# Optimization experiments

Hardware: AMD Instinct MI355X
Metric: run time of the kernel (lower is better)

Reference implementation:

```python
import jax, jax.numpy as jnp
import numpy as np

ND, NS = 50000, 30000
FD = FS = 256
H = 256
E = 1000000
EL = 200000


def _lin_init(key, fan_in, fan_out):
    # torch Linear default: U(-1/sqrt(fan_in), 1/sqrt(fan_in)) for W and b
    kw, kb = jax.random.split(key)
    bound = 1.0 / np.sqrt(fan_in)
    W = jax.random.uniform(kw, (fan_in, fan_out), jnp.float32, -bound, bound)
    b = jax.random.uniform(kb, (fan_out,), jnp.float32, -bound, bound)
    return W, b


def setup_inputs() -> dict:
    key = jax.random.key(0)
    ks = jax.random.split(key, 16)
    x_drug = jax.random.normal(ks[0], (ND, FD), jnp.float32)
    x_disease = jax.random.normal(ks[1], (NS, FS), jnp.float32)
    edge_src = jax.random.randint(ks[2], (E,), 0, ND, jnp.int64)
    edge_dst = jax.random.randint(ks[3], (E,), 0, NS, jnp.int64)
    label_row = jax.random.randint(ks[4], (EL,), 0, ND, jnp.int64)
    label_col = jax.random.randint(ks[5], (EL,), 0, NS, jnp.int64)
    # SAGEConv params per layer per edge type: lin_l (on aggregated src, with bias),
    # lin_r (on dst root, no bias). Edge types: ds = drug->disease, sd = disease->drug (rev).
    Wl1_ds, bl1_ds = _lin_init(ks[6], FD, H)
    Wr1_ds, _ = _lin_init(ks[7], FS, H)
    Wl1_sd, bl1_sd = _lin_init(ks[8], FS, H)
    Wr1_sd, _ = _lin_init(ks[9], FD, H)
    Wl2_ds, bl2_ds = _lin_init(ks[10], H, H)
    Wr2_ds, _ = _lin_init(ks[11], H, H)
    Wl2_sd, bl2_sd = _lin_init(ks[12], H, H)
    Wr2_sd, _ = _lin_init(ks[13], H, H)
    Wdec1, bdec1 = _lin_init(ks[14], 2 * H, H)
    Wdec2, bdec2 = _lin_init(ks[15], H, 1)
    return dict(x_drug=x_drug, x_disease=x_disease,
                edge_src=edge_src, edge_dst=edge_dst,
                label_row=label_row, label_col=label_col,
                Wl1_ds=Wl1_ds, bl1_ds=bl1_ds, Wr1_ds=Wr1_ds,
                Wl1_sd=Wl1_sd, bl1_sd=bl1_sd, Wr1_sd=Wr1_sd,
                Wl2_ds=Wl2_ds, bl2_ds=bl2_ds, Wr2_ds=Wr2_ds,
                Wl2_sd=Wl2_sd, bl2_sd=bl2_sd, Wr2_sd=Wr2_sd,
                Wdec1=Wdec1, bdec1=bdec1, Wdec2=Wdec2, bdec2=bdec2)


def _mean_agg(x_src, src, dst, n_dst):
    # gather source features per edge, mean-scatter into destinations
    msg = x_src[src]                                         # [E, F]
    s = jax.ops.segment_sum(msg, dst, num_segments=n_dst)    # [n_dst, F]
    cnt = jax.ops.segment_sum(jnp.ones_like(dst, x_src.dtype), dst, num_segments=n_dst)
    return s / jnp.maximum(cnt, 1.0)[:, None]


def _sage_layer(x_drug, x_dis, src, dst,
                Wl_ds, bl_ds, Wr_ds, Wl_sd, bl_sd, Wr_sd):
    z_dis = _mean_agg(x_drug, src, dst, NS) @ Wl_ds + bl_ds + x_dis @ Wr_ds
    z_drug = _mean_agg(x_dis, dst, src, ND) @ Wl_sd + bl_sd + x_drug @ Wr_sd
    return z_drug, z_dis


def reference(x_drug, x_disease, edge_src, edge_dst, label_row, label_col,
              Wl1_ds, bl1_ds, Wr1_ds, Wl1_sd, bl1_sd, Wr1_sd,
              Wl2_ds, bl2_ds, Wr2_ds, Wl2_sd, bl2_sd, Wr2_sd,
              Wdec1, bdec1, Wdec2, bdec2):
    # layer 1 (relu)
    zd, zs = _sage_layer(x_drug, x_disease, edge_src, edge_dst,
                         Wl1_ds, bl1_ds, Wr1_ds, Wl1_sd, bl1_sd, Wr1_sd)
    zd, zs = jax.nn.relu(zd), jax.nn.relu(zs)
    # layer 2 (no relu, last layer)
    zd, zs = _sage_layer(zd, zs, edge_src, edge_dst,
                         Wl2_ds, bl2_ds, Wr2_ds, Wl2_sd, bl2_sd, Wr2_sd)
    # edge decoder
    z = jnp.concatenate([zd[label_row], zs[label_col]], axis=-1)  # [EL, 2H]
    h = jax.nn.relu(z @ Wdec1 + bdec1)
    out = (h @ Wdec2 + bdec2).reshape(-1)
    return out
```

## Files before the change

kernel.cpp:

```cpp
#include <hip/hip_runtime.h>
#include <hip/hip_bf16.h>

#define ND 50000
#define NS 30000
#define NE 1000000
#define EL 200000
#define NTOT (NS + ND)
#define SCAN_BLK ((NTOT + 1023) / 1024)

#define RANK_BLKS ((NE + 255) / 256)
#define CONV_BLKS 20000
#define TRW4_BLKS 1024
#define COMP_BLKS 64
#define BIAS_BLKS 2
#define MEGA_BLKS (RANK_BLKS + CONV_BLKS + TRW4_BLKS + COMP_BLKS + BIAS_BLKS)

typedef short short8 __attribute__((ext_vector_type(8)));
typedef float f32x4 __attribute__((ext_vector_type(4)));

__device__ __forceinline__ float b2f(unsigned short u) {
    union { unsigned int i; float f; } c; c.i = ((unsigned int)u) << 16; return c.f;
}
__device__ __forceinline__ unsigned short f2b(float f) {
    __hip_bfloat16 h = __float2bfloat16(f);
    union { __hip_bfloat16 h; unsigned short u; } c; c.h = h; return c.u;
}

__device__ __forceinline__ void gload_lds16(const unsigned short* g, unsigned short* l) {
    __builtin_amdgcn_global_load_lds(
        (const __attribute__((address_space(1))) unsigned int*)g,
        (__attribute__((address_space(3))) unsigned int*)l, 16, 0, 0);
}

struct WAll {
    const float* w1[4];
    const float* w2[4];
    const float* wdec1;
    const float* bl2_ds;
    const float* bl2_sd;
};

__global__ void zero_kernel(int* a, int n) {
    int i = blockIdx.x * blockDim.x + threadIdx.x;
    if (i < n) a[i] = 0;
}

__global__ __launch_bounds__(256) void mega_prep(const int* __restrict__ esrc,
                                                 const int* __restrict__ edst,
                                                 int* cnt_drug, int* cnt_dis,
                                                 unsigned short* __restrict__ rank_sd,
                                                 unsigned short* __restrict__ rank_ds,
                                                 const float* __restrict__ xd,
                                                 const float* __restrict__ xs,
                                                 unsigned short* __restrict__ xd_b,
                                                 unsigned short* __restrict__ xs_b,
                                                 WAll wa,
                                                 unsigned short* __restrict__ Wt,
                                                 float* __restrict__ cbuf) {
    __shared__ float w2t[16][256];
    const int b = blockIdx.x, t = threadIdx.x;
    if (b < RANK_BLKS) {
        int i = b * 256 + t;
        if (i < NE) {
            int s = esrc[i], d = edst[i];
            rank_ds[i] = (unsigned short)atomicAdd(&cnt_dis[d], 1);
            rank_sd[i] = (unsigned short)atomicAdd(&cnt_drug[s], 1);
        }
    } else if (b < RANK_BLKS + CONV_BLKS) {
        int i = ((b - RANK_BLKS) * 256 + t) * 4;
        const int NDE = ND * 256;
        if (i < NDE) {
            float4 v = *reinterpret_cast<const float4*>(xd + i);
            ushort4 o; o.x = f2b(v.x); o.y = f2b(v.y); o.z = f2b(v.z); o.w = f2b(v.w);
            *reinterpret_cast<ushort4*>(xd_b + i) = o;
        } else {
            int j = i - NDE;
            float4 v = *reinterpret_cast<const float4*>(xs + j);
            ushort4 o; o.x = f2b(v.x); o.y = f2b(v.y); o.z = f2b(v.z); o.w = f2b(v.w);
            *reinterpret_cast<ushort4*>(xs_b + j) = o;
        }
    } else if (b < RANK_BLKS + CONV_BLKS + TRW4_BLKS) {
        int o = (b - RANK_BLKS - CONV_BLKS) * 256 + t;
        int mat = o >> 16, idx = o & 65535;
        int n = idx >> 8, k = idx & 255;
        Wt[o] = f2b(wa.w1[mat][k * 256 + n]);
    } else if (b < RANK_BLKS + CONV_BLKS + TRW4_BLKS + COMP_BLKS) {
        int cb = b - RANK_BLKS - CONV_BLKS - TRW4_BLKS;
        int mat = cb >> 4;
        int k0 = (cb & 15) * 16;
        const float* W2 = wa.w2[mat];
        const float* Wd = wa.wdec1 + ((mat < 2) ? 65536 : 0);
        for (int idx = t; idx < 4096; idx += 256) {
            int r = idx >> 8, c = idx & 255;
            w2t[r][c] = W2[(k0 + r) * 256 + c];
        }
        __syncthreads();
        float acc[16] = {};
        const int n = t;
        for (int j = 0; j < 256; ++j) {
            float wd = Wd[j * 256 + n];
#pragma unroll
            for (int k = 0; k < 16; ++k) acc[k] += w2t[k][j] * wd;
        }
        unsigned short* dst = Wt + (size_t)(4 + mat) * 65536 + n * 256 + k0;
#pragma unroll
        for (int k = 0; k < 16; ++k) dst[k] = f2b(acc[k]);
    } else {
        int bb = b - RANK_BLKS - CONV_BLKS - TRW4_BLKS - COMP_BLKS;
        const float* bsrc = bb ? wa.bl2_sd : wa.bl2_ds;
        const float* Wd = wa.wdec1 + (bb ? 0 : 65536);
        float acc = 0.f;
        const int n = t;
        for (int j = 0; j < 256; ++j) acc += bsrc[j] * Wd[j * 256 + n];
        cbuf[bb * 256 + n] = acc;
    }
}


__global__ __launch_bounds__(256) void scan_part(const int* __restrict__ cnt,
                                                 int* __restrict__ bsum) {
    __shared__ int red[4];
    int t = threadIdx.x, lane = t & 63, wid = t >> 6;
    int base = blockIdx.x * 1024 + t * 4;
    int s = 0;
    if (base < NTOT) {
        int4 c = *reinterpret_cast<const int4*>(cnt + base);
        s = c.x + c.y + c.z + c.w;
    }
#pragma unroll
    for (int off = 32; off; off >>= 1) s += __shfl_down(s, off);
    if (lane == 0) red[wid] = s;
    __syncthreads();
    if (t == 0) bsum[blockIdx.x] = red[0] + red[1] + red[2] + red[3];
}

__global__ void scan_top(int* bsum, int nb) {
    int lane = threadIdx.x;
    int a0 = lane < nb ? bsum[lane] : 0;
    int a1 = (64 + lane) < nb ? bsum[64 + lane] : 0;
    int i0 = a0, i1 = a1;
#pragma unroll
    for (int off = 1; off < 64; off <<= 1) {
        int t0 = __shfl_up(i0, off);
        int t1 = __shfl_up(i1, off);
        if (lane >= off) { i0 += t0; i1 += t1; }
    }
    int tot0 = __shfl(i0, 63);
    if (lane < nb) bsum[lane] = i0 - a0;
    if (64 + lane < nb) bsum[64 + lane] = tot0 + i1 - a1;
}

__global__ __launch_bounds__(256) void scan_emit(const int* __restrict__ cnt,
                                                 const int* __restrict__ boff,
                                                 int* __restrict__ row_dis,
                                                 int* __restrict__ row_drug,
                                                 float* __restrict__ inv_dis,
                                                 float* __restrict__ inv_drug) {
    __shared__ int wsum[4];
    int t = threadIdx.x, lane = t & 63, wid = t >> 6;
    int base = blockIdx.x * 1024 + t * 4;
    int4 c = make_int4(0, 0, 0, 0);
    if (base < NTOT) c = *reinterpret_cast<const int4*>(cnt + base);
    int sl = c.x + c.y + c.z + c.w;
    int sc = sl;
#pragma unroll
    for (int off = 1; off < 64; off <<= 1) {
        int tv = __shfl_up(sc, off);
        if (lane >= off) sc += tv;
    }
    if (lane == 63) wsum[wid] = sc;
    __syncthreads();
    int woff = 0;
    for (int w2 = 0; w2 < wid; ++w2) woff += wsum[w2];
    int run = boff[blockIdx.x] + woff + (sc - sl);
    int cc[4] = { c.x, c.y, c.z, c.w };
    if (base < NTOT) {
#pragma unroll
        for (int k = 0; k < 4; ++k) {
            int i = base + k;
            float iv = 1.0f / (float)(cc[k] > 1 ? cc[k] : 1);
            if (i < NS) { row_dis[i] = run; inv_dis[i] = iv; }
            else        { row_drug[i - NS] = run - NE; inv_drug[i - NS] = iv; }
            run += cc[k];
        }
    }
    if (blockIdx.x == 0 && t == 0) { row_dis[NS] = NE; row_drug[ND] = NE; }
}

__global__ void place_kernel(const int* __restrict__ src, const int* __restrict__ dst,
                             const int* __restrict__ row_drug, const int* __restrict__ row_dis,
                             const unsigned short* __restrict__ rank_sd,
                             const unsigned short* __restrict__ rank_ds,
                             unsigned short* __restrict__ val_sd,
                             unsigned short* __restrict__ val_ds, int n) {
    int i = blockIdx.x * blockDim.x + threadIdx.x;
    if (i < n) {
        int s = src[i], d = dst[i];
        val_ds[row_dis[d] + (int)rank_ds[i]] = (unsigned short)s;
        val_sd[row_drug[s] + (int)rank_sd[i]] = (unsigned short)d;
    }
}


__global__ __launch_bounds__(256) void agg_bf2(const unsigned short* __restrict__ srcDis,
                                               const unsigned short* __restrict__ srcDrug,
                                               const int* __restrict__ row_dis,
                                               const int* __restrict__ row_drug,
                                               const unsigned short* __restrict__ val_ds,
                                               const unsigned short* __restrict__ val_sd,
                                               const float* __restrict__ inv_dis,
                                               const float* __restrict__ inv_drug,
                                               unsigned short* __restrict__ outDis,
                                               unsigned short* __restrict__ outDrug) {
    int wid = threadIdx.x >> 6, lane = threadIdx.x & 63;
    int node = blockIdx.x * 4 + wid;
    const int half = lane >> 5;
    const int sub = lane & 31;
    const unsigned short* xsrc; const int* row; const unsigned short* vals;
    const float* inv; unsigned short* outp;
    if (node < NS) {
        xsrc = srcDis; row = row_dis; vals = val_ds; inv = inv_dis; outp = outDis;
    } else {
        node -= NS;
        if (node >= ND) return;
        xsrc = srcDrug; row = row_drug; vals = val_sd; inv = inv_drug; outp = outDrug;
    }
    const int beg = row[node], end = row[node + 1];
    const int off = sub * 8;
    float a[8] = {};
    int j = beg;
    for (; j + 8 <= end; j += 8) {
        int r0 = vals[j     + half];
        int r1 = vals[j + 2 + half];
        int r2 = vals[j + 4 + half];
        int r3 = vals[j + 6 + half];
        short8 v0 = *reinterpret_cast<const short8*>(xsrc + r0 * 256 + off);
        short8 v1 = *reinterpret_cast<const short8*>(xsrc + r1 * 256 + off);
        short8 v2 = *reinterpret_cast<const short8*>(xsrc + r2 * 256 + off);
        short8 v3 = *reinterpret_cast<const short8*>(xsrc + r3 * 256 + off);
#pragma unroll
        for (int k = 0; k < 8; ++k)
            a[k] += b2f((unsigned short)v0[k]) + b2f((unsigned short)v1[k])
                  + b2f((unsigned short)v2[k]) + b2f((unsigned short)v3[k]);
    }
    for (; j + 2 <= end; j += 2) {
        int r = vals[j + half];
        short8 v = *reinterpret_cast<const short8*>(xsrc + r * 256 + off);
#pragma unroll
        for (int k = 0; k < 8; ++k) a[k] += b2f((unsigned short)v[k]);
    }
    if (j < end && half == 0) {
        int r = vals[j];
        short8 v = *reinterpret_cast<const short8*>(xsrc + r * 256 + off);
#pragma unroll
        for (int k = 0; k < 8; ++k) a[k] += b2f((unsigned short)v[k]);
    }
#pragma unroll
    for (int k = 0; k < 8; ++k) a[k] += __shfl_xor(a[k], 32);
    if (half == 0) {
        const float iv = inv[node];
        short8 o;
#pragma unroll
        for (int k = 0; k < 8; ++k) o[k] = (short)f2b(a[k] * iv);
        *reinterpret_cast<short8*>(outp + node * 256 + off) = o;
    }
}


struct GemmSeg {
    const unsigned short* A1;
    const unsigned short* A2;
    const unsigned short* B1t;
    const unsigned short* B2t;
    const float* bias;
    unsigned short* C;
    int M; int relu; int nblk; int nsteps;
};

__global__ __launch_bounds__(256) void gemm_lds(GemmSeg sa, GemmSeg sb) {
    __shared__ unsigned short As[128 * 64];
    __shared__ unsigned short Bs[128 * 64];
    GemmSeg s;
    int bx = blockIdx.x;
    if (bx < sa.nblk) s = sa;
    else { s = sb; bx -= sa.nblk; }

    const int t = threadIdx.x;
    const int lane = t & 63, w = t >> 6;
    const int wr = w >> 1, wc = w & 1;
    const int fr = lane & 15, g = lane >> 4;
    const int bm0 = bx * 128;
    const int n0b = (int)blockIdx.y * 128;
    const int M = s.M;
    const int r8 = lane >> 3, slotL = lane & 7;

    f32x4 acc[4][4];
#pragma unroll
    for (int m = 0; m < 4; ++m)
#pragma unroll
        for (int n = 0; n < 4; ++n)
            acc[m][n] = (f32x4){0.f, 0.f, 0.f, 0.f};

    for (int st = 0; st < s.nsteps; ++st) {
        const int k0 = (st & 3) * 64;
        const unsigned short* Ap = (st & 4) ? s.A2 : s.A1;
        const unsigned short* Bp = (st & 4) ? s.B2t : s.B1t;
#pragma unroll
        for (int j = 0; j < 4; ++j) {
            const int is = w * 4 + j;
            const int row = is * 8 + r8;
            const int sl = slotL ^ (row & 7);
            int ra = bm0 + row; if (ra >= M) ra = M - 1;
            gload_lds16(Ap + (size_t)ra * 256 + k0 + sl * 8, &As[is * 512]);
            gload_lds16(Bp + (size_t)(n0b + row) * 256 + k0 + sl * 8, &Bs[is * 512]);
        }
        __syncthreads();
#pragma unroll
        for (int kc = 0; kc < 2; ++kc) {
            const int q = kc * 4 + g;
            short8 a[4], b[4];
#pragma unroll
            for (int n = 0; n < 4; ++n) {
                const int br = wc * 64 + n * 16 + fr;
                b[n] = *reinterpret_cast<const short8*>(&Bs[br * 64 + (q ^ (fr & 7)) * 8]);
            }
#pragma unroll
            for (int m = 0; m < 4; ++m) {
                const int ar = wr * 64 + m * 16 + fr;
                a[m] = *reinterpret_cast<const short8*>(&As[ar * 64 + (q ^ (fr & 7)) * 8]);
            }
#pragma unroll
            for (int m = 0; m < 4; ++m)
#pragma unroll
                for (int n = 0; n < 4; ++n)
                    acc[m][n] = __builtin_amdgcn_mfma_f32_16x16x32_bf16(a[m], b[n], acc[m][n], 0, 0, 0);
        }
        __syncthreads();
    }

#pragma unroll
    for (int n = 0; n < 4; ++n) {
        const int col = n0b + wc * 64 + n * 16 + fr;
        const float bv = s.bias ? s.bias[col] : 0.0f;
#pragma unroll
        for (int m = 0; m < 4; ++m) {
#pragma unroll
            for (int r = 0; r < 4; ++r) {
                int row = bm0 + wr * 64 + m * 16 + g * 4 + r;
                if (row < M) {
                    float v = acc[m][n][r] + bv;
                    if (s.relu) v = fmaxf(v, 0.f);
                    s.C[row * 256 + col] = f2b(v);
                }
            }
        }
    }
}


__global__ __launch_bounds__(256) void dec_edge(const unsigned short* __restrict__ Pd,
                                                const unsigned short* __restrict__ Ps,
                                                const int* __restrict__ lrow,
                                                const int* __restrict__ lcol,
                                                const float* __restrict__ b1,
                                                const float* __restrict__ w2,
                                                const float* __restrict__ b2,
                                                float* __restrict__ outp, int n) {
    int wid = threadIdx.x >> 6, lane = threadIdx.x & 63;
    int half = lane >> 5, sl = lane & 31;
    int e = blockIdx.x * 8 + wid * 2 + half;
    if (e >= n) return;
    int r = lrow[e], c = lcol[e];
    const int off = sl * 8;
    short8 pd = *reinterpret_cast<const short8*>(Pd + r * 256 + off);
    short8 ps = *reinterpret_cast<const short8*>(Ps + c * 256 + off);
    float s = 0.f;
#pragma unroll
    for (int k = 0; k < 8; ++k) {
        float h = b2f((unsigned short)pd[k]) + b2f((unsigned short)ps[k]) + b1[off + k];
        s += fmaxf(h, 0.f) * w2[off + k];
    }
#pragma unroll
    for (int o = 16; o; o >>= 1) s += __shfl_down(s, o, 32);
    if (sl == 0) outp[e] = s + b2[0];
}


extern "C" void kernel_launch(void* const* d_in, const int* in_sizes, int n_in,
                              void* d_out, int out_size, void* d_ws, size_t ws_size,
                              hipStream_t stream) {
    const float* x_drug = (const float*)d_in[0];
    const float* x_dis  = (const float*)d_in[1];
    const int* esrc = (const int*)d_in[2];
    const int* edst = (const int*)d_in[3];
    const int* lrow = (const int*)d_in[4];
    const int* lcol = (const int*)d_in[5];
    const float* Wl1_ds = (const float*)d_in[6];
    const float* bl1_ds = (const float*)d_in[7];
    const float* Wr1_ds = (const float*)d_in[8];
    const float* Wl1_sd = (const float*)d_in[9];
    const float* bl1_sd = (const float*)d_in[10];
    const float* Wr1_sd = (const float*)d_in[11];
    const float* Wl2_ds = (const float*)d_in[12];
    const float* bl2_ds = (const float*)d_in[13];
    const float* Wr2_ds = (const float*)d_in[14];
    const float* Wl2_sd = (const float*)d_in[15];
    const float* bl2_sd = (const float*)d_in[16];
    const float* Wr2_sd = (const float*)d_in[17];
    const float* Wdec1 = (const float*)d_in[18];
    const float* bdec1 = (const float*)d_in[19];
    const float* Wdec2 = (const float*)d_in[20];
    const float* bdec2 = (const float*)d_in[21];
    float* outp = (float*)d_out;

    char* ws = (char*)d_ws;
    size_t off = 0;
    auto alloc = [&](size_t bytes) -> void* {
        void* p = ws + off;
        off = (off + bytes + 255) & ~(size_t)255;
        return p;
    };
    int* cnt       = (int*)alloc((size_t)NTOT * 4);
    int* bsum      = (int*)alloc((size_t)SCAN_BLK * 4);
    int* row_dis   = (int*)alloc((size_t)(NS + 1) * 4);
    int* row_drug  = (int*)alloc((size_t)(ND + 1) * 4);
    float* inv_dis = (float*)alloc((size_t)NS * 4);
    float* inv_drug= (float*)alloc((size_t)ND * 4);
    float* cbuf    = (float*)alloc((size_t)512 * 4);
    unsigned short* rank_ds = (unsigned short*)alloc((size_t)NE * 2);
    unsigned short* rank_sd = (unsigned short*)alloc((size_t)NE * 2);
    unsigned short* val_ds  = (unsigned short*)alloc((size_t)NE * 2);
    unsigned short* val_sd  = (unsigned short*)alloc((size_t)NE * 2);
    unsigned short* Wt   = (unsigned short*)alloc((size_t)8 * 65536 * 2);
    unsigned short* xd_b = (unsigned short*)alloc((size_t)ND * 256 * 2);
    unsigned short* xs_b = (unsigned short*)alloc((size_t)NS * 256 * 2);
    unsigned short* aggs = (unsigned short*)alloc((size_t)NS * 256 * 2);
    unsigned short* aggd = (unsigned short*)alloc((size_t)ND * 256 * 2);
    unsigned short* zd1  = (unsigned short*)alloc((size_t)ND * 256 * 2);
    unsigned short* zs1  = (unsigned short*)alloc((size_t)NS * 256 * 2);
    unsigned short* Pd   = (unsigned short*)alloc((size_t)ND * 256 * 2);
    unsigned short* Ps   = (unsigned short*)alloc((size_t)NS * 256 * 2);
    int* cnt_dis = cnt;
    int* cnt_drug = cnt + NS;

    zero_kernel<<<(NTOT + 255) / 256, 256, 0, stream>>>(cnt, NTOT);

    WAll wa;
    wa.w1[0] = Wl1_ds; wa.w1[1] = Wr1_ds; wa.w1[2] = Wl1_sd; wa.w1[3] = Wr1_sd;
    wa.w2[0] = Wl2_ds; wa.w2[1] = Wr2_ds; wa.w2[2] = Wl2_sd; wa.w2[3] = Wr2_sd;
    wa.wdec1 = Wdec1; wa.bl2_ds = bl2_ds; wa.bl2_sd = bl2_sd;
    mega_prep<<<MEGA_BLKS, 256, 0, stream>>>(esrc, edst, cnt_drug, cnt_dis,
                                             rank_sd, rank_ds,
                                             x_drug, x_dis, xd_b, xs_b,
                                             wa, Wt, cbuf);
    unsigned short* WT[8];
    for (int i = 0; i < 8; ++i) WT[i] = Wt + (size_t)i * 65536;

    scan_part<<<SCAN_BLK, 256, 0, stream>>>(cnt, bsum);
    scan_top<<<1, 64, 0, stream>>>(bsum, SCAN_BLK);
    scan_emit<<<SCAN_BLK, 256, 0, stream>>>(cnt, bsum, row_dis, row_drug, inv_dis, inv_drug);
    place_kernel<<<(NE + 255) / 256, 256, 0, stream>>>(esrc, edst, row_drug, row_dis,
                                                       rank_sd, rank_ds, val_sd, val_ds, NE);

    const int AGG_GRID = (NTOT + 3) / 4;
    const int NB_NS = (NS + 127) / 128, NB_ND = (ND + 127) / 128;
    dim3 gemm_grid(NB_NS + NB_ND, 2);

    agg_bf2<<<AGG_GRID, 256, 0, stream>>>(xd_b, xs_b, row_dis, row_drug, val_ds, val_sd,
                                          inv_dis, inv_drug, aggs, aggd);
    {
        GemmSeg a = { aggs, xs_b, WT[0], WT[1], bl1_ds, zs1, NS, 1, NB_NS, 8 };
        GemmSeg b = { aggd, xd_b, WT[2], WT[3], bl1_sd, zd1, ND, 1, NB_ND, 8 };
        gemm_lds<<<gemm_grid, 256, 0, stream>>>(a, b);
    }

    agg_bf2<<<AGG_GRID, 256, 0, stream>>>(zd1, zs1, row_dis, row_drug, val_ds, val_sd,
                                          inv_dis, inv_drug, aggs, aggd);
    {
        GemmSeg a = { aggs, zs1, WT[4], WT[5], cbuf,       Ps, NS, 0, NB_NS, 8 };
        GemmSeg b = { aggd, zd1, WT[6], WT[7], cbuf + 256, Pd, ND, 0, NB_ND, 8 };
        gemm_lds<<<gemm_grid, 256, 0, stream>>>(a, b);
    }

    dec_edge<<<(EL + 7) / 8, 256, 0, stream>>>(Pd, Ps, lrow, lcol, bdec1, Wdec2, bdec2, outp, EL);
}
```

Measured before the change: 532.4 us.

## Privatize degree-count atomics per XCC and fold them with prefix offsets

Edge degree counting now uses eight per-XCC copies of the count array, chosen by reading the hardware XCC id, so atomics stay local to one die's L2 and avoid cross-die contention. A new fold kernel sums the copies and writes per-XCC prefix offsets, and the place kernel adds that offset to the encoded local rank. This costs an 8x larger zeroing pass, an extra kernel, and extra reads during placement, and it relies on the per-XCC local rank fitting in 13 bits. Separately, the shared-memory staging in the weight-composition branch is removed in favour of direct global reads.

```diff
diff --git a/kernel.cpp b/kernel.cpp
--- a/kernel.cpp
+++ b/kernel.cpp
@@ -47,7 +47,7 @@
 
 __global__ __launch_bounds__(256) void mega_prep(const int* __restrict__ esrc,
                                                  const int* __restrict__ edst,
-                                                 int* cnt_drug, int* cnt_dis,
+                                                 int* __restrict__ cnt8,
                                                  unsigned short* __restrict__ rank_sd,
                                                  unsigned short* __restrict__ rank_ds,
                                                  const float* __restrict__ xd,
@@ -57,14 +57,19 @@
                                                  WAll wa,
                                                  unsigned short* __restrict__ Wt,
                                                  float* __restrict__ cbuf) {
-    __shared__ float w2t[16][256];
     const int b = blockIdx.x, t = threadIdx.x;
     if (b < RANK_BLKS) {
+        unsigned xcc;
+        asm volatile("s_getreg_b32 %0, hwreg(HW_REG_XCC_ID)" : "=s"(xcc));
+        xcc &= 7;
+        int* cbase = cnt8 + (size_t)xcc * NTOT;
         int i = b * 256 + t;
         if (i < NE) {
             int s = esrc[i], d = edst[i];
-            rank_ds[i] = (unsigned short)atomicAdd(&cnt_dis[d], 1);
-            rank_sd[i] = (unsigned short)atomicAdd(&cnt_drug[s], 1);
+            int ld = atomicAdd(&cbase[d], 1);
+            int ls = atomicAdd(&cbase[NS + s], 1);
+            rank_ds[i] = (unsigned short)((xcc << 13) | ld);
+            rank_sd[i] = (unsigned short)((xcc << 13) | ls);
         }
     } else if (b < RANK_BLKS + CONV_BLKS) {
         int i = ((b - RANK_BLKS) * 256 + t) * 4;
@@ -81,38 +86,51 @@
         }
     } else if (b < RANK_BLKS + CONV_BLKS + TRW4_BLKS) {
         int o = (b - RANK_BLKS - CONV_BLKS) * 256 + t;
-        int mat = o >> 16, idx = o & 65535;
-        int n = idx >> 8, k = idx & 255;
+        int mat = o >> 16, i2 = o & 65535;
+        int n = i2 >> 8, k = i2 & 255;
         Wt[o] = f2b(wa.w1[mat][k * 256 + n]);
     } else if (b < RANK_BLKS + CONV_BLKS + TRW4_BLKS + COMP_BLKS) {
-        int cb = b - RANK_BLKS - CONV_BLKS - TRW4_BLKS;
-        int mat = cb >> 4;
-        int k0 = (cb & 15) * 16;
+        int idx = b - RANK_BLKS - CONV_BLKS - TRW4_BLKS;
+        int mat = idx >> 4;
+        int k0 = (idx & 15) * 16;
         const float* W2 = wa.w2[mat];
         const float* Wd = wa.wdec1 + ((mat < 2) ? 65536 : 0);
-        for (int idx = t; idx < 4096; idx += 256) {
-            int r = idx >> 8, c = idx & 255;
-            w2t[r][c] = W2[(k0 + r) * 256 + c];
-        }
-        __syncthreads();
         float acc[16] = {};
         const int n = t;
         for (int j = 0; j < 256; ++j) {
             float wd = Wd[j * 256 + n];
 #pragma unroll
-            for (int k = 0; k < 16; ++k) acc[k] += w2t[k][j] * wd;
+            for (int k = 0; k < 16; ++k) acc[k] += W2[(k0 + k) * 256 + j] * wd;
         }
         unsigned short* dst = Wt + (size_t)(4 + mat) * 65536 + n * 256 + k0;
 #pragma unroll
         for (int k = 0; k < 16; ++k) dst[k] = f2b(acc[k]);
     } else {
-        int bb = b - RANK_BLKS - CONV_BLKS - TRW4_BLKS - COMP_BLKS;
-        const float* bsrc = bb ? wa.bl2_sd : wa.bl2_ds;
-        const float* Wd = wa.wdec1 + (bb ? 0 : 65536);
+        int idx = b - RANK_BLKS - CONV_BLKS - TRW4_BLKS - COMP_BLKS;
+        const float* bsrc = idx ? wa.bl2_sd : wa.bl2_ds;
+        const float* Wd = wa.wdec1 + (idx ? 0 : 65536);
         float acc = 0.f;
         const int n = t;
         for (int j = 0; j < 256; ++j) acc += bsrc[j] * Wd[j * 256 + n];
-        cbuf[bb * 256 + n] = acc;
+        cbuf[idx * 256 + n] = acc;
+    }
+}
+
+__global__ __launch_bounds__(256) void fold8(const int* __restrict__ cnt8,
+                                             int* __restrict__ pre,
+                                             int* __restrict__ cnt) {
+    int i = blockIdx.x * 256 + threadIdx.x;
+    if (i < NTOT) {
+        int run = 0;
+        int p[8];
+#pragma unroll
+        for (int x = 0; x < 8; ++x) {
+            p[x] = run;
+            run += cnt8[(size_t)x * NTOT + i];
+        }
+#pragma unroll
+        for (int x = 0; x < 8; ++x) pre[(size_t)i * 8 + x] = p[x];
+        cnt[i] = run;
     }
 }
 
@@ -189,6 +207,7 @@
 
 __global__ void place_kernel(const int* __restrict__ src, const int* __restrict__ dst,
                              const int* __restrict__ row_drug, const int* __restrict__ row_dis,
+                             const int* __restrict__ pre,
                              const unsigned short* __restrict__ rank_sd,
                              const unsigned short* __restrict__ rank_ds,
                              unsigned short* __restrict__ val_sd,
@@ -196,8 +215,9 @@
     int i = blockIdx.x * blockDim.x + threadIdx.x;
     if (i < n) {
         int s = src[i], d = dst[i];
-        val_ds[row_dis[d] + (int)rank_ds[i]] = (unsigned short)s;
-        val_sd[row_drug[s] + (int)rank_sd[i]] = (unsigned short)d;
+        int rd = rank_ds[i], rs = rank_sd[i];
+        val_ds[row_dis[d] + pre[(size_t)d * 8 + (rd >> 13)] + (rd & 8191)] = (unsigned short)s;
+        val_sd[row_drug[s] + pre[(size_t)(NS + s) * 8 + (rs >> 13)] + (rs & 8191)] = (unsigned short)d;
     }
 }
 
@@ -421,6 +441,8 @@
         return p;
     };
     int* cnt       = (int*)alloc((size_t)NTOT * 4);
+    int* cnt8      = (int*)alloc((size_t)8 * NTOT * 4);
+    int* pre       = (int*)alloc((size_t)8 * NTOT * 4);
     int* bsum      = (int*)alloc((size_t)SCAN_BLK * 4);
     int* row_dis   = (int*)alloc((size_t)(NS + 1) * 4);
     int* row_drug  = (int*)alloc((size_t)(ND + 1) * 4);
@@ -440,26 +462,25 @@
     unsigned short* zs1  = (unsigned short*)alloc((size_t)NS * 256 * 2);
     unsigned short* Pd   = (unsigned short*)alloc((size_t)ND * 256 * 2);
     unsigned short* Ps   = (unsigned short*)alloc((size_t)NS * 256 * 2);
-    int* cnt_dis = cnt;
-    int* cnt_drug = cnt + NS;
-
-    zero_kernel<<<(NTOT + 255) / 256, 256, 0, stream>>>(cnt, NTOT);
+
+    zero_kernel<<<(8 * NTOT + 255) / 256, 256, 0, stream>>>(cnt8, 8 * NTOT);
 
     WAll wa;
     wa.w1[0] = Wl1_ds; wa.w1[1] = Wr1_ds; wa.w1[2] = Wl1_sd; wa.w1[3] = Wr1_sd;
     wa.w2[0] = Wl2_ds; wa.w2[1] = Wr2_ds; wa.w2[2] = Wl2_sd; wa.w2[3] = Wr2_sd;
     wa.wdec1 = Wdec1; wa.bl2_ds = bl2_ds; wa.bl2_sd = bl2_sd;
-    mega_prep<<<MEGA_BLKS, 256, 0, stream>>>(esrc, edst, cnt_drug, cnt_dis,
+    mega_prep<<<MEGA_BLKS, 256, 0, stream>>>(esrc, edst, cnt8,
                                              rank_sd, rank_ds,
                                              x_drug, x_dis, xd_b, xs_b,
                                              wa, Wt, cbuf);
     unsigned short* WT[8];
     for (int i = 0; i < 8; ++i) WT[i] = Wt + (size_t)i * 65536;
 
+    fold8<<<(NTOT + 255) / 256, 256, 0, stream>>>(cnt8, pre, cnt);
     scan_part<<<SCAN_BLK, 256, 0, stream>>>(cnt, bsum);
     scan_top<<<1, 64, 0, stream>>>(bsum, SCAN_BLK);
     scan_emit<<<SCAN_BLK, 256, 0, stream>>>(cnt, bsum, row_dis, row_drug, inv_dis, inv_drug);
-    place_kernel<<<(NE + 255) / 256, 256, 0, stream>>>(esrc, edst, row_drug, row_dis,
+    place_kernel<<<(NE + 255) / 256, 256, 0, stream>>>(esrc, edst, row_drug, row_dis, pre,
                                                        rank_sd, rank_ds, val_sd, val_ds, NE);
 
     const int AGG_GRID = (NTOT + 3) / 4;
```

Result: slower. 561.7 us (+5.5%).
